# Kernel optimization log

Hardware: AMD Instinct MI355X
Metric: run time of the kernel (lower is better)

Reference implementation:

```python
import jax, jax.numpy as jnp
import numpy as np

L = 24
D = 2048
NUM_BLOCKS = 8
EPS = 1e-6
B, T = 2, 1024


def _block_layout(num_layers, num_blocks):
    base = num_layers // num_blocks
    rem = num_layers % num_blocks
    sizes = [base] * num_blocks
    if rem:
        sizes[-1] += rem
    starts = list(np.cumsum([0] + sizes[:-1]))
    return sizes, starts


def _rmsnorm(x, weight, eps=EPS):
    # x: (..., d)
    var = jnp.mean(x * x, axis=-1, keepdims=True)
    return x * jax.lax.rsqrt(var + eps) * weight


def setup_inputs() -> dict:
    key = jax.random.key(0)
    k1, k2, k3 = jax.random.split(key, 3)
    layer_outputs = jax.random.normal(k1, (L, B, T, D), dtype=jnp.float32)
    embedding = jax.random.normal(k2, (B, T, D), dtype=jnp.float32)
    queries = jax.random.normal(k3, (L, D), dtype=jnp.float32) * 0.02
    key_norm_weight = jnp.ones((D,), dtype=jnp.float32)
    return {
        "layer_outputs": layer_outputs,
        "embedding": embedding,
        "queries": queries,
        "key_norm_weight": key_norm_weight,
    }


def reference(layer_outputs, embedding, queries, key_norm_weight):
    """Faithful port of BlockAttnRes.compute_all_inputs.

    layer_outputs: (L, B, T, d)  -- f_l(h_l) for each layer
    embedding:     (B, T, d)     -- b_0
    queries:       (L, d)        -- zero-init pseudo-queries (randn here)
    key_norm_weight: (d,)        -- RMSNorm scale
    Returns (L, B, T, d): AttnRes input h_l for each layer.
    """
    num_layers = layer_outputs.shape[0]
    sizes, starts = _block_layout(num_layers, NUM_BLOCKS)

    block_reprs = [embedding]
    partial = None
    inputs = []
    block_n = 0
    for l in range(num_layers):  # fixed structural loop over layers
        # advance block index
        while l >= starts[block_n] + sizes[block_n]:
            block_n += 1
        i = l - starts[block_n]
        sources = list(block_reprs)
        if i > 0 and partial is not None:
            sources.append(partial)
        v_stack = jnp.stack(sources, axis=2)            # (B, T, n, d)
        k_stack = _rmsnorm(v_stack, key_norm_weight)    # (B, T, n, d)
        scores = jnp.einsum("btnd,d->btn", k_stack, queries[l])
        alpha = jax.nn.softmax(scores, axis=-1)         # (B, T, n)
        h = jnp.einsum("btn,btnd->btd", alpha, v_stack)
        inputs.append(h)
        f_l = layer_outputs[l]
        partial = f_l if partial is None else partial + f_l
        if i + 1 >= sizes[block_n]:
            block_reprs.append(partial)
            partial = None
    return jnp.stack(inputs, axis=0)  # (L, B, T, d)
```

## Files before the change

kernel.cpp:

```cpp
#include <hip/hip_runtime.h>
#include <hip/hip_bf16.h>

constexpr int LAYERS = 24;
constexpr int DIM    = 2048;
constexpr int NBLK   = 8;
constexpr float EPSV = 1e-6f;
constexpr int TPB    = 512;
constexpr int EPT    = 4;
constexpr int NSLOT  = 147;

typedef float vf4 __attribute__((ext_vector_type(4)));

__device__ constexpr int OFF_TAB[24] =
    {0,1,4,7,10,14,18,22,27,32,37,43,49,55,62,69,76,84,92,100,109,118,127,137};
__device__ constexpr int SSQS[7] = {9,21,36,54,75,99,126};

__device__ __forceinline__ unsigned pk2(float a, float b) {
    __hip_bfloat162 h2(__float2bfloat16(a), __float2bfloat16(b));
    union { __hip_bfloat162 h; unsigned u; } c; c.h = h2; return c.u;
}
__device__ __forceinline__ float upk(unsigned p, int hi) {
    union { unsigned u; float f; } c;
    c.u = hi ? (p & 0xffff0000u) : (p << 16);
    return c.f;
}

__global__ void prep_qw_kernel(const float* __restrict__ q,
                               const float* __restrict__ w,
                               float* __restrict__ qw, int n) {
    int idx = blockIdx.x * blockDim.x + threadIdx.x;
    if (idx < n) qw[idx] = q[idx] * w[idx & (DIM - 1)];
}

template<bool PREMUL>
__global__ void __launch_bounds__(TPB, 4)
block_attn_res_kernel(const float* __restrict__ lo,
                      const float* __restrict__ emb,
                      const float* __restrict__ q1,
                      const float* __restrict__ wgt,
                      float* __restrict__ out,
                      int bt_total)
{
    const int bt   = blockIdx.x;
    const int tid  = threadIdx.x;
    const int lane = tid & 63;
    const int wid  = tid >> 6;
    const int grp  = (wid << 2) | (lane >> 4);
    const int c0   = tid * 4;

    __shared__ float red[32][NSLOT + 1];
    __shared__ float redJ[NSLOT + 1];
    __shared__ float ab[LAYERS][12];

    const float invD = 1.f / (float)DIM;
    const size_t lstride = (size_t)bt_total * DIM;
    const float* lop = lo + (size_t)bt * DIM + c0;

    auto wred = [&](float x, int slot) {
        x += __shfl_xor(x, 1);
        x += __shfl_xor(x, 2);
        x += __shfl_xor(x, 4);
        x += __shfl_xor(x, 8);
        if ((lane & 15) == 0) red[grp][slot] = x;
    };

    float wv[EPT];
    if (!PREMUL) {
        vf4 w0 = *reinterpret_cast<const vf4*>(wgt + c0);
        wv[0]=w0.x; wv[1]=w0.y; wv[2]=w0.z; wv[3]=w0.w;
    }

    float e[EPT];
    {
        vf4 v0 = __builtin_nontemporal_load(
            reinterpret_cast<const vf4*>(emb + (size_t)bt * DIM + c0));
        e[0]=v0.x; e[1]=v0.y; e[2]=v0.z; e[3]=v0.w;
    }

    unsigned fpk[LAYERS-1][EPT/2];
    unsigned Spk[NBLK-1][EPT/2];
    float part[EPT];

    {
        vf4 u0 = __builtin_nontemporal_load(reinterpret_cast<const vf4*>(lop));
        part[0]=u0.x; part[1]=u0.y; part[2]=u0.z; part[3]=u0.w;
        fpk[0][0] = pk2(part[0], part[1]);
        fpk[0][1] = pk2(part[2], part[3]);

        vf4 w0; w0.x=e[0]; w0.y=e[1]; w0.z=e[2]; w0.w=e[3];
        *reinterpret_cast<vf4*>(out + (size_t)bt * DIM + c0) = w0;

        float sq = e[0]*e[0] + e[1]*e[1] + e[2]*e[2] + e[3]*e[3];
        wred(sq, 0);
    }

    float fb[2][EPT], qb[2][EPT];
    {
        vf4 u1 = __builtin_nontemporal_load(
            reinterpret_cast<const vf4*>(lop + 1 * lstride));
        fb[1][0]=u1.x; fb[1][1]=u1.y; fb[1][2]=u1.z; fb[1][3]=u1.w;
        vf4 q1v = *reinterpret_cast<const vf4*>(q1 + (size_t)1 * DIM + c0);
        qb[1][0]=q1v.x; qb[1][1]=q1v.y; qb[1][2]=q1v.z; qb[1][3]=q1v.w;

        vf4 u2 = __builtin_nontemporal_load(
            reinterpret_cast<const vf4*>(lop + 2 * lstride));
        fb[0][0]=u2.x; fb[0][1]=u2.y; fb[0][2]=u2.z; fb[0][3]=u2.w;
        vf4 q2v = *reinterpret_cast<const vf4*>(q1 + (size_t)2 * DIM + c0);
        qb[0][0]=q2v.x; qb[0][1]=q2v.y; qb[0][2]=q2v.z; qb[0][3]=q2v.w;
    }

    #pragma unroll
    for (int l = 1; l < LAYERS; ++l) {
        const int m   = l / 3;
        const int i   = l - 3 * m;
        const int off = OFF_TAB[l];
        const int p   = l & 1;

        float qwv[EPT];
        #pragma unroll
        for (int j = 0; j < EPT; ++j)
            qwv[j] = PREMUL ? qb[p][j] : qb[p][j] * wv[j];
        float fC[EPT];
        if (l < LAYERS - 1) {
            #pragma unroll
            for (int j = 0; j < EPT; ++j) fC[j] = fb[p][j];
        }

        if (l + 2 <= LAYERS - 2) {
            vf4 u0 = __builtin_nontemporal_load(
                reinterpret_cast<const vf4*>(lop + (size_t)(l + 2) * lstride));
            fb[p][0]=u0.x; fb[p][1]=u0.y; fb[p][2]=u0.z; fb[p][3]=u0.w;
        }
        if (l + 2 <= LAYERS - 1) {
            vf4 v0 = *reinterpret_cast<const vf4*>(q1 + (size_t)(l + 2) * DIM + c0);
            qb[p][0]=v0.x; qb[p][1]=v0.y; qb[p][2]=v0.z; qb[p][3]=v0.w;
        }

        {
            float dv = e[0]*qwv[0] + e[1]*qwv[1] + e[2]*qwv[2] + e[3]*qwv[3];
            wred(dv, off);
        }
        #pragma unroll
        for (int s = 0; s < NBLK - 1; ++s) {
            if (s < m) {
                float dv;
                if (s == m - 1 && i == 0) {
                    dv = part[0]*qwv[0] + part[1]*qwv[1]
                       + part[2]*qwv[2] + part[3]*qwv[3];
                } else {
                    dv = upk(Spk[s][0],0)*qwv[0] + upk(Spk[s][0],1)*qwv[1]
                       + upk(Spk[s][1],0)*qwv[2] + upk(Spk[s][1],1)*qwv[3];
                }
                wred(dv, off + 1 + s);
            }
        }
        if (i > 0) {
            float dv = part[0]*qwv[0] + part[1]*qwv[1]
                     + part[2]*qwv[2] + part[3]*qwv[3];
            float sq = part[0]*part[0] + part[1]*part[1]
                     + part[2]*part[2] + part[3]*part[3];
            wred(dv, off + m + 1);
            wred(sq, off + m + 2);
        } else {
            float sq = part[0]*part[0] + part[1]*part[1]
                     + part[2]*part[2] + part[3]*part[3];
            wred(sq, off + m + 1);
        }

        if (l < LAYERS - 1) {
            if (i == 0) {
                #pragma unroll
                for (int j = 0; j < EPT; ++j) part[j] = fC[j];
            } else {
                #pragma unroll
                for (int j = 0; j < EPT; ++j) part[j] += fC[j];
            }
            fpk[l][0] = pk2(fC[0], fC[1]);
            fpk[l][1] = pk2(fC[2], fC[3]);
            if (i == 2 && m < NBLK - 1) {
                Spk[m][0] = pk2(part[0], part[1]);
                Spk[m][1] = pk2(part[2], part[3]);
            }
        }
    }

    __syncthreads();

    if (tid < NSLOT) {
        float t = 0.f;
        #pragma unroll
        for (int g = 0; g < 32; ++g) t += red[g][tid];
        redJ[tid] = t;
    }
    __syncthreads();

    if (tid >= 1 && tid < LAYERS) {
        const int l = tid;
        const int m = l / 3;
        const int i = l - 3 * m;
        const int off = OFF_TAB[l];
        const float ssqe = redJ[0];
        float sce = redJ[off] * rsqrtf(ssqe * invD + EPSV);
        float mx = sce;
        float scS[NBLK - 1];
        #pragma unroll
        for (int s = 0; s < NBLK - 1; ++s) {
            if (s < m) {
                scS[s] = redJ[off + 1 + s] * rsqrtf(redJ[SSQS[s]] * invD + EPSV);
                mx = fmaxf(mx, scS[s]);
            }
        }
        float scp = 0.f;
        if (i > 0) {
            scp = redJ[off + m + 1] * rsqrtf(redJ[off + m + 2] * invD + EPSV);
            mx = fmaxf(mx, scp);
        }
        float ee = __expf(sce - mx), den = ee;
        float es[NBLK - 1];
        #pragma unroll
        for (int s = 0; s < NBLK - 1; ++s) {
            es[s] = (s < m) ? __expf(scS[s] - mx) : 0.f;
            den += es[s];
        }
        float ep = 0.f;
        if (i > 0) { ep = __expf(scp - mx); den += ep; }
        const float inv = 1.f / den;
        ab[l][0] = ee * inv;
        #pragma unroll
        for (int s = 0; s < NBLK - 1; ++s)
            if (s < m) ab[l][1 + s] = es[s] * inv;
        if (i > 0) ab[l][1 + m] = ep * inv;
    }
    __syncthreads();

    part[0] = upk(fpk[0][0],0); part[1] = upk(fpk[0][0],1);
    part[2] = upk(fpk[0][1],0); part[3] = upk(fpk[0][1],1);

    #pragma unroll
    for (int l = 1; l < LAYERS; ++l) {
        const int m = l / 3;
        const int i = l - 3 * m;

        float h[EPT];
        {
            const float a0 = ab[l][0];
            #pragma unroll
            for (int j = 0; j < EPT; ++j) h[j] = a0 * e[j];
        }
        #pragma unroll
        for (int s = 0; s < NBLK - 1; ++s) {
            if (s < m) {
                const float a = ab[l][1 + s];
                h[0] += a * upk(Spk[s][0],0);
                h[1] += a * upk(Spk[s][0],1);
                h[2] += a * upk(Spk[s][1],0);
                h[3] += a * upk(Spk[s][1],1);
            }
        }
        if (i > 0) {
            const float a = ab[l][1 + m];
            #pragma unroll
            for (int j = 0; j < EPT; ++j) h[j] += a * part[j];
        }

        {
            vf4 w0; w0.x=h[0]; w0.y=h[1]; w0.z=h[2]; w0.w=h[3];
            *reinterpret_cast<vf4*>(out + ((size_t)l * bt_total + bt) * DIM + c0) = w0;
        }

        if (l < LAYERS - 1) {
            if (i == 0) {
                part[0] = upk(fpk[l][0],0); part[1] = upk(fpk[l][0],1);
                part[2] = upk(fpk[l][1],0); part[3] = upk(fpk[l][1],1);
            } else {
                part[0] += upk(fpk[l][0],0); part[1] += upk(fpk[l][0],1);
                part[2] += upk(fpk[l][1],0); part[3] += upk(fpk[l][1],1);
            }
        }
    }
}

extern "C" void kernel_launch(void* const* d_in, const int* in_sizes, int n_in,
                              void* d_out, int out_size, void* d_ws, size_t ws_size,
                              hipStream_t stream) {
    const float* lo  = (const float*)d_in[0];
    const float* emb = (const float*)d_in[1];
    const float* qry = (const float*)d_in[2];
    const float* wgt = (const float*)d_in[3];
    float* outp = (float*)d_out;

    const int bt_total = in_sizes[1] / DIM;
    const int nq = in_sizes[2];

    if (ws_size >= (size_t)nq * sizeof(float)) {
        float* qwbuf = (float*)d_ws;
        prep_qw_kernel<<<(nq + 255) / 256, 256, 0, stream>>>(qry, wgt, qwbuf, nq);
        block_attn_res_kernel<true><<<bt_total, TPB, 0, stream>>>(
            lo, emb, qwbuf, nullptr, outp, bt_total);
    } else {
        block_attn_res_kernel<false><<<bt_total, TPB, 0, stream>>>(
            lo, emb, qry, wgt, outp, bt_total);
    }
}
```

Baseline: 209.9 us.

## Process two tokens per block and deepen layer-output prefetch to four

Each workgroup now loops over two consecutive (b,t) rows instead of one, halving the grid so all blocks fit in a single residency wave. The layer-output prefetch ring grows from two to four slots so more global loads are in flight per thread. The reduction scratch row stride is also padded by one more float. The intent is to hide memory latency better in this bandwidth-bound kernel. The cost is higher register pressure and serialized per-block work, which could lower occupancy or overlap between tokens.

```diff
diff --git a/kernel.cpp b/kernel.cpp
--- a/kernel.cpp
+++ b/kernel.cpp
@@ -8,6 +8,8 @@
 constexpr int TPB    = 512;
 constexpr int EPT    = 4;
 constexpr int NSLOT  = 147;
+constexpr int RSTR   = NSLOT + 2;
+constexpr int NBT    = 2;
 
 typedef float vf4 __attribute__((ext_vector_type(4)));
 
@@ -41,20 +43,18 @@
                       float* __restrict__ out,
                       int bt_total)
 {
-    const int bt   = blockIdx.x;
     const int tid  = threadIdx.x;
     const int lane = tid & 63;
     const int wid  = tid >> 6;
     const int grp  = (wid << 2) | (lane >> 4);
     const int c0   = tid * 4;
 
-    __shared__ float red[32][NSLOT + 1];
+    __shared__ float red[32][RSTR];
     __shared__ float redJ[NSLOT + 1];
     __shared__ float ab[LAYERS][12];
 
     const float invD = 1.f / (float)DIM;
     const size_t lstride = (size_t)bt_total * DIM;
-    const float* lop = lo + (size_t)bt * DIM + c0;
 
     auto wred = [&](float x, int slot) {
         x += __shfl_xor(x, 1);
@@ -70,211 +70,221 @@
         wv[0]=w0.x; wv[1]=w0.y; wv[2]=w0.z; wv[3]=w0.w;
     }
 
-    float e[EPT];
-    {
-        vf4 v0 = __builtin_nontemporal_load(
-            reinterpret_cast<const vf4*>(emb + (size_t)bt * DIM + c0));
-        e[0]=v0.x; e[1]=v0.y; e[2]=v0.z; e[3]=v0.w;
-    }
-
-    unsigned fpk[LAYERS-1][EPT/2];
-    unsigned Spk[NBLK-1][EPT/2];
-    float part[EPT];
-
-    {
-        vf4 u0 = __builtin_nontemporal_load(reinterpret_cast<const vf4*>(lop));
-        part[0]=u0.x; part[1]=u0.y; part[2]=u0.z; part[3]=u0.w;
-        fpk[0][0] = pk2(part[0], part[1]);
-        fpk[0][1] = pk2(part[2], part[3]);
-
-        vf4 w0; w0.x=e[0]; w0.y=e[1]; w0.z=e[2]; w0.w=e[3];
-        *reinterpret_cast<vf4*>(out + (size_t)bt * DIM + c0) = w0;
-
-        float sq = e[0]*e[0] + e[1]*e[1] + e[2]*e[2] + e[3]*e[3];
-        wred(sq, 0);
-    }
-
-    float fb[2][EPT], qb[2][EPT];
-    {
-        vf4 u1 = __builtin_nontemporal_load(
-            reinterpret_cast<const vf4*>(lop + 1 * lstride));
-        fb[1][0]=u1.x; fb[1][1]=u1.y; fb[1][2]=u1.z; fb[1][3]=u1.w;
-        vf4 q1v = *reinterpret_cast<const vf4*>(q1 + (size_t)1 * DIM + c0);
-        qb[1][0]=q1v.x; qb[1][1]=q1v.y; qb[1][2]=q1v.z; qb[1][3]=q1v.w;
-
-        vf4 u2 = __builtin_nontemporal_load(
-            reinterpret_cast<const vf4*>(lop + 2 * lstride));
-        fb[0][0]=u2.x; fb[0][1]=u2.y; fb[0][2]=u2.z; fb[0][3]=u2.w;
-        vf4 q2v = *reinterpret_cast<const vf4*>(q1 + (size_t)2 * DIM + c0);
-        qb[0][0]=q2v.x; qb[0][1]=q2v.y; qb[0][2]=q2v.z; qb[0][3]=q2v.w;
-    }
-
-    #pragma unroll
-    for (int l = 1; l < LAYERS; ++l) {
-        const int m   = l / 3;
-        const int i   = l - 3 * m;
-        const int off = OFF_TAB[l];
-        const int p   = l & 1;
-
-        float qwv[EPT];
+    for (int t = 0; t < NBT; ++t) {
+        const int bt = blockIdx.x * NBT + t;
+        if (bt >= bt_total) break;
+        const float* lop = lo + (size_t)bt * DIM + c0;
+
+        float e[EPT];
+        {
+            vf4 v0 = __builtin_nontemporal_load(
+                reinterpret_cast<const vf4*>(emb + (size_t)bt * DIM + c0));
+            e[0]=v0.x; e[1]=v0.y; e[2]=v0.z; e[3]=v0.w;
+        }
+
+        unsigned fpk[LAYERS-1][EPT/2];
+        unsigned Spk[NBLK-1][EPT/2];
+        float part[EPT];
+
+        {
+            vf4 u0 = __builtin_nontemporal_load(reinterpret_cast<const vf4*>(lop));
+            part[0]=u0.x; part[1]=u0.y; part[2]=u0.z; part[3]=u0.w;
+            fpk[0][0] = pk2(part[0], part[1]);
+            fpk[0][1] = pk2(part[2], part[3]);
+
+            vf4 w0; w0.x=e[0]; w0.y=e[1]; w0.z=e[2]; w0.w=e[3];
+            *reinterpret_cast<vf4*>(out + (size_t)bt * DIM + c0) = w0;
+
+            float sq = e[0]*e[0] + e[1]*e[1] + e[2]*e[2] + e[3]*e[3];
+            wred(sq, 0);
+        }
+
+        float fb[4][EPT], qb[2][EPT];
+        {
+            vf4 u;
+            u = __builtin_nontemporal_load(reinterpret_cast<const vf4*>(lop + 1 * lstride));
+            fb[1][0]=u.x; fb[1][1]=u.y; fb[1][2]=u.z; fb[1][3]=u.w;
+            u = __builtin_nontemporal_load(reinterpret_cast<const vf4*>(lop + 2 * lstride));
+            fb[2][0]=u.x; fb[2][1]=u.y; fb[2][2]=u.z; fb[2][3]=u.w;
+            u = __builtin_nontemporal_load(reinterpret_cast<const vf4*>(lop + 3 * lstride));
+            fb[3][0]=u.x; fb[3][1]=u.y; fb[3][2]=u.z; fb[3][3]=u.w;
+            u = __builtin_nontemporal_load(reinterpret_cast<const vf4*>(lop + 4 * lstride));
+            fb[0][0]=u.x; fb[0][1]=u.y; fb[0][2]=u.z; fb[0][3]=u.w;
+            vf4 q;
+            q = *reinterpret_cast<const vf4*>(q1 + (size_t)1 * DIM + c0);
+            qb[1][0]=q.x; qb[1][1]=q.y; qb[1][2]=q.z; qb[1][3]=q.w;
+            q = *reinterpret_cast<const vf4*>(q1 + (size_t)2 * DIM + c0);
+            qb[0][0]=q.x; qb[0][1]=q.y; qb[0][2]=q.z; qb[0][3]=q.w;
+        }
+
         #pragma unroll
-        for (int j = 0; j < EPT; ++j)
-            qwv[j] = PREMUL ? qb[p][j] : qb[p][j] * wv[j];
-        float fC[EPT];
-        if (l < LAYERS - 1) {
-            #pragma unroll
-            for (int j = 0; j < EPT; ++j) fC[j] = fb[p][j];
-        }
-
-        if (l + 2 <= LAYERS - 2) {
-            vf4 u0 = __builtin_nontemporal_load(
-                reinterpret_cast<const vf4*>(lop + (size_t)(l + 2) * lstride));
-            fb[p][0]=u0.x; fb[p][1]=u0.y; fb[p][2]=u0.z; fb[p][3]=u0.w;
-        }
-        if (l + 2 <= LAYERS - 1) {
-            vf4 v0 = *reinterpret_cast<const vf4*>(q1 + (size_t)(l + 2) * DIM + c0);
-            qb[p][0]=v0.x; qb[p][1]=v0.y; qb[p][2]=v0.z; qb[p][3]=v0.w;
-        }
-
-        {
-            float dv = e[0]*qwv[0] + e[1]*qwv[1] + e[2]*qwv[2] + e[3]*qwv[3];
-            wred(dv, off);
-        }
+        for (int l = 1; l < LAYERS; ++l) {
+            const int m   = l / 3;
+            const int i   = l - 3 * m;
+            const int off = OFF_TAB[l];
+            const int pf  = l & 3;
+            const int pq  = l & 1;
+
+            float qwv[EPT];
+            #pragma unroll
+            for (int j = 0; j < EPT; ++j)
+                qwv[j] = PREMUL ? qb[pq][j] : qb[pq][j] * wv[j];
+            float fC[EPT];
+            if (l < LAYERS - 1) {
+                #pragma unroll
+                for (int j = 0; j < EPT; ++j) fC[j] = fb[pf][j];
+            }
+
+            if (l + 4 <= LAYERS - 2) {
+                vf4 u0 = __builtin_nontemporal_load(
+                    reinterpret_cast<const vf4*>(lop + (size_t)(l + 4) * lstride));
+                fb[pf][0]=u0.x; fb[pf][1]=u0.y; fb[pf][2]=u0.z; fb[pf][3]=u0.w;
+            }
+            if (l + 2 <= LAYERS - 1) {
+                vf4 v0 = *reinterpret_cast<const vf4*>(q1 + (size_t)(l + 2) * DIM + c0);
+                qb[pq][0]=v0.x; qb[pq][1]=v0.y; qb[pq][2]=v0.z; qb[pq][3]=v0.w;
+            }
+
+            {
+                float dv = e[0]*qwv[0] + e[1]*qwv[1] + e[2]*qwv[2] + e[3]*qwv[3];
+                wred(dv, off);
+            }
+            #pragma unroll
+            for (int s = 0; s < NBLK - 1; ++s) {
+                if (s < m) {
+                    float dv;
+                    if (s == m - 1 && i == 0) {
+                        dv = part[0]*qwv[0] + part[1]*qwv[1]
+                           + part[2]*qwv[2] + part[3]*qwv[3];
+                    } else {
+                        dv = upk(Spk[s][0],0)*qwv[0] + upk(Spk[s][0],1)*qwv[1]
+                           + upk(Spk[s][1],0)*qwv[2] + upk(Spk[s][1],1)*qwv[3];
+                    }
+                    wred(dv, off + 1 + s);
+                }
+            }
+            if (i > 0) {
+                float dv = part[0]*qwv[0] + part[1]*qwv[1]
+                         + part[2]*qwv[2] + part[3]*qwv[3];
+                float sq = part[0]*part[0] + part[1]*part[1]
+                         + part[2]*part[2] + part[3]*part[3];
+                wred(dv, off + m + 1);
+                wred(sq, off + m + 2);
+            } else {
+                float sq = part[0]*part[0] + part[1]*part[1]
+                         + part[2]*part[2] + part[3]*part[3];
+                wred(sq, off + m + 1);
+            }
+
+            if (l < LAYERS - 1) {
+                if (i == 0) {
+                    #pragma unroll
+                    for (int j = 0; j < EPT; ++j) part[j] = fC[j];
+                } else {
+                    #pragma unroll
+                    for (int j = 0; j < EPT; ++j) part[j] += fC[j];
+                }
+                fpk[l][0] = pk2(fC[0], fC[1]);
+                fpk[l][1] = pk2(fC[2], fC[3]);
+                if (i == 2 && m < NBLK - 1) {
+                    Spk[m][0] = pk2(part[0], part[1]);
+                    Spk[m][1] = pk2(part[2], part[3]);
+                }
+            }
+        }
+
+        __syncthreads();
+
+        if (tid < NSLOT) {
+            float s = 0.f;
+            #pragma unroll
+            for (int g = 0; g < 32; ++g) s += red[g][tid];
+            redJ[tid] = s;
+        }
+        __syncthreads();
+
+        if (tid >= 1 && tid < LAYERS) {
+            const int l = tid;
+            const int m = l / 3;
+            const int i = l - 3 * m;
+            const int off = OFF_TAB[l];
+            const float ssqe = redJ[0];
+            float sce = redJ[off] * rsqrtf(ssqe * invD + EPSV);
+            float mx = sce;
+            float scS[NBLK - 1];
+            #pragma unroll
+            for (int s = 0; s < NBLK - 1; ++s) {
+                if (s < m) {
+                    scS[s] = redJ[off + 1 + s] * rsqrtf(redJ[SSQS[s]] * invD + EPSV);
+                    mx = fmaxf(mx, scS[s]);
+                }
+            }
+            float scp = 0.f;
+            if (i > 0) {
+                scp = redJ[off + m + 1] * rsqrtf(redJ[off + m + 2] * invD + EPSV);
+                mx = fmaxf(mx, scp);
+            }
+            float ee = __expf(sce - mx), den = ee;
+            float es[NBLK - 1];
+            #pragma unroll
+            for (int s = 0; s < NBLK - 1; ++s) {
+                es[s] = (s < m) ? __expf(scS[s] - mx) : 0.f;
+                den += es[s];
+            }
+            float ep = 0.f;
+            if (i > 0) { ep = __expf(scp - mx); den += ep; }
+            const float inv = 1.f / den;
+            ab[l][0] = ee * inv;
+            #pragma unroll
+            for (int s = 0; s < NBLK - 1; ++s)
+                if (s < m) ab[l][1 + s] = es[s] * inv;
+            if (i > 0) ab[l][1 + m] = ep * inv;
+        }
+        __syncthreads();
+
+        part[0] = upk(fpk[0][0],0); part[1] = upk(fpk[0][0],1);
+        part[2] = upk(fpk[0][1],0); part[3] = upk(fpk[0][1],1);
+
         #pragma unroll
-        for (int s = 0; s < NBLK - 1; ++s) {
-            if (s < m) {
-                float dv;
-                if (s == m - 1 && i == 0) {
-                    dv = part[0]*qwv[0] + part[1]*qwv[1]
-                       + part[2]*qwv[2] + part[3]*qwv[3];
+        for (int l = 1; l < LAYERS; ++l) {
+            const int m = l / 3;
+            const int i = l - 3 * m;
+
+            float h[EPT];
+            {
+                const float a0 = ab[l][0];
+                #pragma unroll
+                for (int j = 0; j < EPT; ++j) h[j] = a0 * e[j];
+            }
+            #pragma unroll
+            for (int s = 0; s < NBLK - 1; ++s) {
+                if (s < m) {
+                    const float a = ab[l][1 + s];
+                    h[0] += a * upk(Spk[s][0],0);
+                    h[1] += a * upk(Spk[s][0],1);
+                    h[2] += a * upk(Spk[s][1],0);
+                    h[3] += a * upk(Spk[s][1],1);
+                }
+            }
+            if (i > 0) {
+                const float a = ab[l][1 + m];
+                #pragma unroll
+                for (int j = 0; j < EPT; ++j) h[j] += a * part[j];
+            }
+
+            {
+                vf4 w0; w0.x=h[0]; w0.y=h[1]; w0.z=h[2]; w0.w=h[3];
+                *reinterpret_cast<vf4*>(out + ((size_t)l * bt_total + bt) * DIM + c0) = w0;
+            }
+
+            if (l < LAYERS - 1) {
+                if (i == 0) {
+                    part[0] = upk(fpk[l][0],0); part[1] = upk(fpk[l][0],1);
+                    part[2] = upk(fpk[l][1],0); part[3] = upk(fpk[l][1],1);
                 } else {
-                    dv = upk(Spk[s][0],0)*qwv[0] + upk(Spk[s][0],1)*qwv[1]
-                       + upk(Spk[s][1],0)*qwv[2] + upk(Spk[s][1],1)*qwv[3];
-                }
-                wred(dv, off + 1 + s);
-            }
-        }
-        if (i > 0) {
-            float dv = part[0]*qwv[0] + part[1]*qwv[1]
-                     + part[2]*qwv[2] + part[3]*qwv[3];
-            float sq = part[0]*part[0] + part[1]*part[1]
-                     + part[2]*part[2] + part[3]*part[3];
-            wred(dv, off + m + 1);
-            wred(sq, off + m + 2);
-        } else {
-            float sq = part[0]*part[0] + part[1]*part[1]
-                     + part[2]*part[2] + part[3]*part[3];
-            wred(sq, off + m + 1);
-        }
-
-        if (l < LAYERS - 1) {
-            if (i == 0) {
-                #pragma unroll
-                for (int j = 0; j < EPT; ++j) part[j] = fC[j];
-            } else {
-                #pragma unroll
-                for (int j = 0; j < EPT; ++j) part[j] += fC[j];
-            }
-            fpk[l][0] = pk2(fC[0], fC[1]);
-            fpk[l][1] = pk2(fC[2], fC[3]);
-            if (i == 2 && m < NBLK - 1) {
-                Spk[m][0] = pk2(part[0], part[1]);
-                Spk[m][1] = pk2(part[2], part[3]);
-            }
-        }
-    }
-
-    __syncthreads();
-
-    if (tid < NSLOT) {
-        float t = 0.f;
-        #pragma unroll
-        for (int g = 0; g < 32; ++g) t += red[g][tid];
-        redJ[tid] = t;
-    }
-    __syncthreads();
-
-    if (tid >= 1 && tid < LAYERS) {
-        const int l = tid;
-        const int m = l / 3;
-        const int i = l - 3 * m;
-        const int off = OFF_TAB[l];
-        const float ssqe = redJ[0];
-        float sce = redJ[off] * rsqrtf(ssqe * invD + EPSV);
-        float mx = sce;
-        float scS[NBLK - 1];
-        #pragma unroll
-        for (int s = 0; s < NBLK - 1; ++s) {
-            if (s < m) {
-                scS[s] = redJ[off + 1 + s] * rsqrtf(redJ[SSQS[s]] * invD + EPSV);
-                mx = fmaxf(mx, scS[s]);
-            }
-        }
-        float scp = 0.f;
-        if (i > 0) {
-            scp = redJ[off + m + 1] * rsqrtf(redJ[off + m + 2] * invD + EPSV);
-            mx = fmaxf(mx, scp);
-        }
-        float ee = __expf(sce - mx), den = ee;
-        float es[NBLK - 1];
-        #pragma unroll
-        for (int s = 0; s < NBLK - 1; ++s) {
-            es[s] = (s < m) ? __expf(scS[s] - mx) : 0.f;
-            den += es[s];
-        }
-        float ep = 0.f;
-        if (i > 0) { ep = __expf(scp - mx); den += ep; }
-        const float inv = 1.f / den;
-        ab[l][0] = ee * inv;
-        #pragma unroll
-        for (int s = 0; s < NBLK - 1; ++s)
-            if (s < m) ab[l][1 + s] = es[s] * inv;
-        if (i > 0) ab[l][1 + m] = ep * inv;
-    }
-    __syncthreads();
-
-    part[0] = upk(fpk[0][0],0); part[1] = upk(fpk[0][0],1);
-    part[2] = upk(fpk[0][1],0); part[3] = upk(fpk[0][1],1);
-
-    #pragma unroll
-    for (int l = 1; l < LAYERS; ++l) {
-        const int m = l / 3;
-        const int i = l - 3 * m;
-
-        float h[EPT];
-        {
-            const float a0 = ab[l][0];
-            #pragma unroll
-            for (int j = 0; j < EPT; ++j) h[j] = a0 * e[j];
-        }
-        #pragma unroll
-        for (int s = 0; s < NBLK - 1; ++s) {
-            if (s < m) {
-                const float a = ab[l][1 + s];
-                h[0] += a * upk(Spk[s][0],0);
-                h[1] += a * upk(Spk[s][0],1);
-                h[2] += a * upk(Spk[s][1],0);
-                h[3] += a * upk(Spk[s][1],1);
-            }
-        }
-        if (i > 0) {
-            const float a = ab[l][1 + m];
-            #pragma unroll
-            for (int j = 0; j < EPT; ++j) h[j] += a * part[j];
-        }
-
-        {
-            vf4 w0; w0.x=h[0]; w0.y=h[1]; w0.z=h[2]; w0.w=h[3];
-            *reinterpret_cast<vf4*>(out + ((size_t)l * bt_total + bt) * DIM + c0) = w0;
-        }
-
-        if (l < LAYERS - 1) {
-            if (i == 0) {
-                part[0] = upk(fpk[l][0],0); part[1] = upk(fpk[l][0],1);
-                part[2] = upk(fpk[l][1],0); part[3] = upk(fpk[l][1],1);
-            } else {
-                part[0] += upk(fpk[l][0],0); part[1] += upk(fpk[l][0],1);
-                part[2] += upk(fpk[l][1],0); part[3] += upk(fpk[l][1],1);
+                    part[0] += upk(fpk[l][0],0); part[1] += upk(fpk[l][0],1);
+                    part[2] += upk(fpk[l][1],0); part[3] += upk(fpk[l][1],1);
+                }
             }
         }
     }
@@ -291,14 +301,15 @@
 
     const int bt_total = in_sizes[1] / DIM;
     const int nq = in_sizes[2];
+    const int nblocks = (bt_total + NBT - 1) / NBT;
 
     if (ws_size >= (size_t)nq * sizeof(float)) {
         float* qwbuf = (float*)d_ws;
         prep_qw_kernel<<<(nq + 255) / 256, 256, 0, stream>>>(qry, wgt, qwbuf, nq);
-        block_attn_res_kernel<true><<<bt_total, TPB, 0, stream>>>(
+        block_attn_res_kernel<true><<<nblocks, TPB, 0, stream>>>(
             lo, emb, qwbuf, nullptr, outp, bt_total);
     } else {
-        block_attn_res_kernel<false><<<bt_total, TPB, 0, stream>>>(
+        block_attn_res_kernel<false><<<nblocks, TPB, 0, stream>>>(
             lo, emb, qry, wgt, outp, bt_total);
     }
 }
```

After: 260.7 us. +24.2%, slower.
